# Performance work log

Measured on AMD Instinct MI355X. Metric: run time of the kernel, lower is better.

Reference implementation:

```python
import jax, jax.numpy as jnp
import numpy as np

N_NODES = 100000
N_EDGES = 1600000
D = 128
N_LAYERS = 3
N_GRAPHS = 128


def setup_inputs() -> dict:
    key = jax.random.key(0)
    ks = jax.random.split(key, 8)
    x = jax.random.normal(ks[0], (N_NODES, D), dtype=jnp.float32)
    # stacked GIN-MLP params (all layers are D->D since hidden_dim == in_dim)
    scale = 1.0 / np.sqrt(D)
    W1 = jax.random.normal(ks[1], (N_LAYERS, D, D), dtype=jnp.float32) * scale
    b1 = jax.random.normal(ks[2], (N_LAYERS, D), dtype=jnp.float32) * 0.01
    W2 = jax.random.normal(ks[3], (N_LAYERS, D, D), dtype=jnp.float32) * scale
    b2 = jax.random.normal(ks[4], (N_LAYERS, D), dtype=jnp.float32) * 0.01
    edge_index = jax.random.randint(ks[5], (2, N_EDGES), 0, N_NODES, dtype=jnp.int64)
    batch = jnp.sort(jax.random.randint(ks[6], (N_NODES,), 0, N_GRAPHS, dtype=jnp.int64))
    return {"x": x, "W1": W1, "b1": b1, "W2": W2, "b2": b2,
            "edge_index": edge_index, "batch": batch}


def reference(x, W1, b1, W2, b2, edge_index, batch):
    src = edge_index[0]
    dst = edge_index[1]
    n = x.shape[0]
    eps = jnp.float32(0.0)  # GIN eps (PyG default, not trained)
    for i in range(N_LAYERS):
        # gather neighbor features along edges, scatter-add to destination nodes
        agg = jax.ops.segment_sum(x[src], dst, num_segments=n)  # [N, D]
        h = (1.0 + eps) * x + agg
        h = jax.nn.relu(h @ W1[i] + b1[i])
        x = h @ W2[i] + b2[i]
    # sum-pool readout per graph
    h_G = jax.ops.segment_sum(x, batch, num_segments=N_GRAPHS)  # [G, D]
    return h_G
```

## Files before the change

kernel.cpp:

```cpp
#include <hip/hip_runtime.h>
#include <hip/hip_bf16.h>
#include <stdint.h>

#define N_NODES 100000
#define N_EDGES 1600000
#define DIM 128
#define N_GRAPHS 128
#define LDA 136

#define NBKT 196
#define BCAP 12288
#define BP   10240
#define IDXCAP 2048

typedef unsigned int uint32;
typedef unsigned short ushort16;

typedef __bf16 bf16x8 __attribute__((ext_vector_type(8)));
typedef float fx4 __attribute__((ext_vector_type(4)));

__device__ __forceinline__ float bfLo(uint32 u){ return __builtin_bit_cast(float, (uint32)(u << 16)); }
__device__ __forceinline__ float bfHi(uint32 u){ return __builtin_bit_cast(float, (uint32)(u & 0xFFFF0000u)); }
__device__ __forceinline__ ushort16 f2bf(float f){
  uint32 u = __builtin_bit_cast(uint32, f);
  u = u + 0x7FFFu + ((u >> 16) & 1u);
  return (ushort16)(u >> 16);
}
__device__ __forceinline__ uint32 pack2(float a, float b){
  return (uint32)f2bf(a) | ((uint32)f2bf(b) << 16);
}

__global__ __launch_bounds__(256) void k_cvt_x(const float* __restrict__ x, ushort16* __restrict__ P,
                                               ushort16* __restrict__ Q){
  if (blockIdx.x == 6250){
    int t = threadIdx.x;
    uint4 z = {0u,0u,0u,0u};
    if (t < 16)                *(uint4*)(P + (size_t)N_NODES*128 + t*8)      = z;
    else if (t < 32)           *(uint4*)(Q + (size_t)N_NODES*128 + (t-16)*8) = z;
    return;
  }
  int idx = (blockIdx.x*256 + threadIdx.x) * 8;
  float4 v0 = *(const float4*)(x + idx);
  float4 v1 = *(const float4*)(x + idx + 4);
  uint4 o;
  o.x = pack2(v0.x, v0.y); o.y = pack2(v0.z, v0.w);
  o.z = pack2(v1.x, v1.y); o.w = pack2(v1.z, v1.w);
  *(uint4*)(P + idx) = o;
}

__global__ __launch_bounds__(256) void k_cvt_w(const float* __restrict__ W1, const float* __restrict__ W2,
                                               ushort16* __restrict__ Wf){
  int tid = blockIdx.x*256 + threadIdx.x;
  int layer = tid >> 12;
  int rem   = tid & 4095;
  int mat   = rem >> 11;
  int nt    = (rem >> 8) & 7;
  int kt    = (rem >> 6) & 3;
  int lane  = rem & 63;
  int kg = lane >> 4, m = lane & 15;
  int n  = nt*16 + m;
  int kb = kt*32 + kg*8;
  const float* src = (mat ? W2 : W1) + layer*16384;
  uint4 o;
  o.x = pack2(src[(kb+0)*128 + n], src[(kb+1)*128 + n]);
  o.y = pack2(src[(kb+2)*128 + n], src[(kb+3)*128 + n]);
  o.z = pack2(src[(kb+4)*128 + n], src[(kb+5)*128 + n]);
  o.w = pack2(src[(kb+6)*128 + n], src[(kb+7)*128 + n]);
  *(uint4*)(Wf + ((((size_t)(layer*2+mat)*8 + nt)*4 + kt)*64 + lane)*8) = o;
}

__global__ __launch_bounds__(512) void k_binA(const int* __restrict__ ei,
                                              int* __restrict__ bucketCursor,
                                              int* __restrict__ temp){
  __shared__ int hist[NBKT];
  __shared__ int base[NBKT];
  __shared__ int gbase[NBKT];
  __shared__ int scanbuf[256];
  __shared__ int sVal[8192];
  __shared__ unsigned short sBkt[8192];
  int t = threadIdx.x;
  int e0 = blockIdx.x * 8192;

  for (int i = t; i < NBKT; i += 512) hist[i] = 0;
  __syncthreads();

  int   myv[16];
  short myb[16];
  short myr[16];
  #pragma unroll
  for (int it = 0; it < 16; ++it){
    int e = e0 + it*512 + t;
    int v = 0; short b = -1; short r = 0;
    if (e < N_EDGES){
      int s = ei[e];
      int d = ei[N_EDGES + e];
      b = (short)(d >> 9);
      v = s | ((d & 511) << 17);
      r = (short)atomicAdd(&hist[b], 1);
    }
    myv[it] = v; myb[it] = b; myr[it] = r;
  }
  __syncthreads();

  if (t < 256) scanbuf[t] = (t < NBKT) ? hist[t] : 0;
  __syncthreads();
  for (int off = 1; off < 256; off <<= 1){
    int x = 0;
    if (t < 256 && t >= off) x = scanbuf[t - off];
    __syncthreads();
    if (t < 256) scanbuf[t] += x;
    __syncthreads();
  }
  if (t < NBKT){
    base[t]  = scanbuf[t] - hist[t];
    gbase[t] = atomicAdd(&bucketCursor[t], hist[t]);
  }
  __syncthreads();

  #pragma unroll
  for (int it = 0; it < 16; ++it){
    if (myb[it] >= 0){
      int p = base[myb[it]] + myr[it];
      sVal[p] = myv[it];
      sBkt[p] = (unsigned short)myb[it];
    }
  }
  __syncthreads();

  int cnt = scanbuf[NBKT - 1];
  for (int p = t; p < cnt; p += 512){
    int b = sBkt[p];
    int g = gbase[b] + (p - base[b]);
    if (g < BCAP) temp[b*BCAP + g] = sVal[p];
  }
}

__global__ __launch_bounds__(512) void k_binB(const int* __restrict__ temp,
                                              const int* __restrict__ bucketCursor,
                                              int* __restrict__ rowptr,
                                              int* __restrict__ rowlen,
                                              int* __restrict__ colx){
  __shared__ int counts[512];
  __shared__ int sc[512];
  __shared__ int cur[512];
  __shared__ int stage[BCAP];
  __shared__ int sorted[BCAP];
  int b = blockIdx.x, t = threadIdx.x;
  int cnt = min(bucketCursor[b], BCAP);
  int gb  = b * BP;
  const int* src = temp + b*BCAP;

  counts[t] = 0;
  __syncthreads();
  for (int p = t; p < cnt; p += 512){
    int v = src[p];
    stage[p] = v;
    atomicAdd(&counts[v >> 17], 1);
  }
  __syncthreads();

  int len  = counts[t];
  int plen = (len + 3) & ~3;
  sc[t] = plen; __syncthreads();
  for (int off = 1; off < 512; off <<= 1){
    int x = (t >= off) ? sc[t - off] : 0; __syncthreads(); sc[t] += x; __syncthreads();
  }
  int excl = sc[t] - plen;
  cur[t] = excl;
  int node = b*512 + t;
  if (node < N_NODES){ rowptr[node] = gb + excl; rowlen[node] = plen; }
  __syncthreads();

  for (int p = t; p < cnt; p += 512){
    int v = stage[p];
    int d = v >> 17;
    int pos = atomicAdd(&cur[d], 1);
    sorted[pos] = v & 0x1FFFF;
  }
  __syncthreads();

  for (int k = len; k < plen; ++k) sorted[excl + k] = N_NODES;
  __syncthreads();

  int total = sc[511];
  for (int p = t; p < total; p += 512) colx[gb + p] = sorted[p];
}

__global__ __launch_bounds__(256, 6) void k_gin(const ushort16* __restrict__ xb, ushort16* __restrict__ hb,
                                                const ushort16* __restrict__ Wt1, const float* __restrict__ b1,
                                                const ushort16* __restrict__ Wt2, const float* __restrict__ b2,
                                                const int* __restrict__ rowptr, const int* __restrict__ rowlen,
                                                const int* __restrict__ colx){
  __shared__ __attribute__((aligned(16))) ushort16 sA[64 * LDA];
  __shared__ __attribute__((aligned(16))) int sIdx[IDXCAP];
  __shared__ int sOff[64];
  __shared__ int sLen[64];

  int t = threadIdx.x;
  int row0 = blockIdx.x * 64;
  int jBase = rowptr[row0];
  int lastV = min(row0 + 63, N_NODES - 1);
  int total = rowptr[lastV] + rowlen[lastV] - jBase;

  if (t < 64){
    int g = row0 + t;
    int off = 0, len = 0;
    if (g < N_NODES){ off = rowptr[g] - jBase; len = rowlen[g]; }
    sOff[t] = off; sLen[t] = len;
  }
  bool fast = (total <= IDXCAP);
  if (fast){
    for (int p = t; p < total; p += 256) sIdx[p] = colx[jBase + p];
  }
  __syncthreads();

  int wave = t >> 6, lane = t & 63;
  int g16 = lane >> 4, o = lane & 15;
  const uint32* xw = (const uint32*)xb;

#define GATH(r) (*(const uint4*)(xw + (size_t)(r)*64 + o*4))
#define ACC8(u) do { \
    a0 += (fx4){ bfLo((u).x), bfHi((u).x), bfLo((u).y), bfHi((u).y) }; \
    a1 += (fx4){ bfLo((u).z), bfHi((u).z), bfLo((u).w), bfHi((u).w) }; \
  } while(0)

  for (int q = 0; q < 4; ++q){
    int ln  = wave*16 + q*4 + g16;
    int off = sOff[ln];
    int len = sLen[ln];
    int gn  = row0 + ln;
    uint4 xv = {0u,0u,0u,0u};
    if (gn < N_NODES) xv = *(const uint4*)(xw + (size_t)gn*64 + o*4);
    fx4 a0 = (fx4){0.f,0.f,0.f,0.f};
    fx4 a1 = (fx4){0.f,0.f,0.f,0.f};

    if (fast){
      int rd = 0;
      for (; rd + 8 <= len; rd += 8){
        int i0 = sIdx[off+rd  ], i1 = sIdx[off+rd+1], i2 = sIdx[off+rd+2], i3 = sIdx[off+rd+3];
        int i4 = sIdx[off+rd+4], i5 = sIdx[off+rd+5], i6 = sIdx[off+rd+6], i7 = sIdx[off+rd+7];
        uint4 u0 = GATH(i0); uint4 u1 = GATH(i1); uint4 u2 = GATH(i2); uint4 u3 = GATH(i3);
        uint4 u4 = GATH(i4); uint4 u5 = GATH(i5); uint4 u6 = GATH(i6); uint4 u7 = GATH(i7);
        ACC8(u0); ACC8(u1); ACC8(u2); ACC8(u3);
        ACC8(u4); ACC8(u5); ACC8(u6); ACC8(u7);
      }
      if (rd < len){
        int i0 = sIdx[off+rd], i1 = sIdx[off+rd+1], i2 = sIdx[off+rd+2], i3 = sIdx[off+rd+3];
        uint4 u0 = GATH(i0); uint4 u1 = GATH(i1); uint4 u2 = GATH(i2); uint4 u3 = GATH(i3);
        ACC8(u0); ACC8(u1); ACC8(u2); ACC8(u3);
      }
    } else {
      for (int rd = 0; rd < len; rd += 4){
        int i0 = colx[jBase+off+rd], i1 = colx[jBase+off+rd+1];
        int i2 = colx[jBase+off+rd+2], i3 = colx[jBase+off+rd+3];
        uint4 u0 = GATH(i0); uint4 u1 = GATH(i1); uint4 u2 = GATH(i2); uint4 u3 = GATH(i3);
        ACC8(u0); ACC8(u1); ACC8(u2); ACC8(u3);
      }
    }

    uint4 r;
    r.x = pack2(a0[0]+bfLo(xv.x), a0[1]+bfHi(xv.x));
    r.y = pack2(a0[2]+bfLo(xv.y), a0[3]+bfHi(xv.y));
    r.z = pack2(a1[0]+bfLo(xv.z), a1[1]+bfHi(xv.z));
    r.w = pack2(a1[2]+bfLo(xv.w), a1[3]+bfHi(xv.w));
    *(uint4*)(sA + ln*LDA + o*8) = r;
  }
#undef GATH
#undef ACC8
  __syncthreads();

  int m = lane & 15, kg = lane >> 4;
  int n0 = wave * 2;

  bf16x8 bfa[4], bfb[4];
  #pragma unroll
  for (int kt = 0; kt < 4; ++kt){
    bfa[kt] = *(const bf16x8*)(Wt1 + (((n0+0)*4 + kt)*64 + lane)*8);
    bfb[kt] = *(const bf16x8*)(Wt1 + (((n0+1)*4 + kt)*64 + lane)*8);
  }

  fx4 acc[4][2];
  #pragma unroll
  for (int mt = 0; mt < 4; ++mt){ acc[mt][0] = (fx4){0,0,0,0}; acc[mt][1] = (fx4){0,0,0,0}; }

  #pragma unroll
  for (int kt = 0; kt < 4; ++kt){
    #pragma unroll
    for (int mt = 0; mt < 4; ++mt){
      bf16x8 av = *(const bf16x8*)(sA + (mt*16 + m)*LDA + kg*8 + kt*32);
      acc[mt][0] = __builtin_amdgcn_mfma_f32_16x16x32_bf16(av, bfa[kt], acc[mt][0], 0, 0, 0);
      acc[mt][1] = __builtin_amdgcn_mfma_f32_16x16x32_bf16(av, bfb[kt], acc[mt][1], 0, 0, 0);
    }
  }
  float bva = b1[(n0+0)*16 + m];
  float bvb = b1[(n0+1)*16 + m];
  __syncthreads();

  #pragma unroll
  for (int mt = 0; mt < 4; ++mt){
    #pragma unroll
    for (int r = 0; r < 4; ++r){
      int row = mt*16 + kg*4 + r;
      sA[row*LDA + (n0+0)*16 + m] = f2bf(fmaxf(acc[mt][0][r] + bva, 0.f));
      sA[row*LDA + (n0+1)*16 + m] = f2bf(fmaxf(acc[mt][1][r] + bvb, 0.f));
    }
  }
  #pragma unroll
  for (int kt = 0; kt < 4; ++kt){
    bfa[kt] = *(const bf16x8*)(Wt2 + (((n0+0)*4 + kt)*64 + lane)*8);
    bfb[kt] = *(const bf16x8*)(Wt2 + (((n0+1)*4 + kt)*64 + lane)*8);
  }
  float cva = b2[(n0+0)*16 + m];
  float cvb = b2[(n0+1)*16 + m];
  #pragma unroll
  for (int mt = 0; mt < 4; ++mt){ acc[mt][0] = (fx4){0,0,0,0}; acc[mt][1] = (fx4){0,0,0,0}; }
  __syncthreads();

  #pragma unroll
  for (int kt = 0; kt < 4; ++kt){
    #pragma unroll
    for (int mt = 0; mt < 4; ++mt){
      bf16x8 av = *(const bf16x8*)(sA + (mt*16 + m)*LDA + kg*8 + kt*32);
      acc[mt][0] = __builtin_amdgcn_mfma_f32_16x16x32_bf16(av, bfa[kt], acc[mt][0], 0, 0, 0);
      acc[mt][1] = __builtin_amdgcn_mfma_f32_16x16x32_bf16(av, bfb[kt], acc[mt][1], 0, 0, 0);
    }
  }

  #pragma unroll
  for (int mt = 0; mt < 4; ++mt){
    #pragma unroll
    for (int r = 0; r < 4; ++r){
      int row = row0 + mt*16 + kg*4 + r;
      if (row < N_NODES){
        hb[row*128 + (n0+0)*16 + m] = f2bf(acc[mt][0][r] + cva);
        hb[row*128 + (n0+1)*16 + m] = f2bf(acc[mt][1][r] + cvb);
      }
    }
  }
}

__device__ __forceinline__ int lower_bound_i(const int* __restrict__ a, int n, int key){
  int lo = 0, hi = n;
  while (lo < hi){ int mid = (lo + hi) >> 1; if (a[mid] < key) lo = mid + 1; else hi = mid; }
  return lo;
}

__global__ __launch_bounds__(256) void k_pool(const ushort16* __restrict__ xb, const int* __restrict__ batch,
                                              float* __restrict__ out){
  int g = blockIdx.x >> 2;
  int p = blockIdx.x & 3;
  int start = lower_bound_i(batch, N_NODES, g);
  int end   = lower_bound_i(batch, N_NODES, g + 1);
  int t = threadIdx.x;
  int c = t & 127;
  int h = t >> 7;
  float acc = 0.f;
  for (int r = start + p*2 + h; r < end; r += 8){
    uint32 u = (uint32)xb[r*128 + c];
    acc += __builtin_bit_cast(float, (uint32)(u << 16));
  }
  __shared__ float red[256];
  red[t] = acc; __syncthreads();
  if (t < 128) atomicAdd(&out[g*128 + c], red[t] + red[t + 128]);
}

extern "C" void kernel_launch(void* const* d_in, const int* in_sizes, int n_in,
                              void* d_out, int out_size, void* d_ws, size_t ws_size,
                              hipStream_t stream) {
  const float* x   = (const float*)d_in[0];
  const float* W1  = (const float*)d_in[1];
  const float* b1  = (const float*)d_in[2];
  const float* W2  = (const float*)d_in[3];
  const float* b2  = (const float*)d_in[4];
  const int*   ei  = (const int*)d_in[5];
  const int*   bat = (const int*)d_in[6];
  float* out = (float*)d_out;

  char* w = (char*)d_ws;
  auto carve = [&](size_t bytes) -> char* {
    char* p = w; w += (bytes + 255) & ~(size_t)255; return p;
  };
  ushort16* P    = (ushort16*)carve((size_t)(N_NODES+1) * DIM * 2);
  ushort16* Q    = (ushort16*)carve((size_t)(N_NODES+1) * DIM * 2);
  ushort16* Wf   = (ushort16*)carve((size_t)3 * 2 * 16384 * 2);
  int* rowptr    = (int*)carve((size_t)N_NODES * 4);
  int* rowlen    = (int*)carve((size_t)N_NODES * 4);
  int* colx      = (int*)carve((size_t)NBKT * BP * 4);
  int* bucketCursor = (int*)carve((NBKT + 1) * 4);
  int* temp      = (int*)Q;

  hipMemsetAsync(bucketCursor, 0, (NBKT + 1) * 4, stream);
  hipMemsetAsync(d_out, 0, (size_t)N_GRAPHS * DIM * 4, stream);

  k_cvt_x<<<6251, 256, 0, stream>>>(x, P, Q);
  k_cvt_w<<<48, 256, 0, stream>>>(W1, W2, Wf);

  k_binA<<<(N_EDGES + 8191)/8192, 512, 0, stream>>>(ei, bucketCursor, temp);
  k_binB<<<NBKT, 512, 0, stream>>>(temp, bucketCursor, rowptr, rowlen, colx);

  const int ginGrid = (N_NODES + 63) / 64;

  k_gin<<<ginGrid, 256, 0, stream>>>(P, Q, Wf + 0*16384, b1 + 0*128, Wf + 1*16384, b2 + 0*128,
                                     rowptr, rowlen, colx);
  k_gin<<<ginGrid, 256, 0, stream>>>(Q, P, Wf + 2*16384, b1 + 1*128, Wf + 3*16384, b2 + 1*128,
                                     rowptr, rowlen, colx);
  k_gin<<<ginGrid, 256, 0, stream>>>(P, Q, Wf + 4*16384, b1 + 2*128, Wf + 5*16384, b2 + 2*128,
                                     rowptr, rowlen, colx);

  k_pool<<<N_GRAPHS * 4, 256, 0, stream>>>(Q, bat, out);
}
```

Before: 372.9 us.

## Fuse x/W conversion and edge binning into one prep kernel, halve bucket size

Merges the x-to-bf16 conversion, weight repacking and first edge-binning pass into a single launch with block-range dispatch, removing two kernel launches and letting the independent work run concurrently. The destination bucketing is also refined from 512-node to 256-node buckets (392 buckets, smaller per-bucket capacity), so the second binning pass has more, smaller blocks with lighter shared-memory use. The trade-offs are smaller overflow headroom per bucket and more global atomics on the bucket cursors.

```diff
diff --git a/kernel.cpp b/kernel.cpp
--- a/kernel.cpp
+++ b/kernel.cpp
@@ -8,10 +8,13 @@
 #define N_GRAPHS 128
 #define LDA 136
 
-#define NBKT 196
-#define BCAP 12288
-#define BP   10240
+#define NBKT 392
+#define BCAP 6144
+#define BP   5632
 #define IDXCAP 2048
+
+#define NBIN_BLK 391
+#define CVT_BLK 3125
 
 typedef unsigned int uint32;
 typedef unsigned short ushort16;
@@ -30,27 +33,99 @@
   return (uint32)f2bf(a) | ((uint32)f2bf(b) << 16);
 }
 
-__global__ __launch_bounds__(256) void k_cvt_x(const float* __restrict__ x, ushort16* __restrict__ P,
-                                               ushort16* __restrict__ Q){
-  if (blockIdx.x == 6250){
-    int t = threadIdx.x;
+__global__ __launch_bounds__(512) void k_prep(const float* __restrict__ x,
+                                              const float* __restrict__ W1, const float* __restrict__ W2,
+                                              const int* __restrict__ ei,
+                                              ushort16* __restrict__ P, ushort16* __restrict__ Q,
+                                              ushort16* __restrict__ Wf,
+                                              int* __restrict__ bucketCursor,
+                                              int* __restrict__ temp){
+  __shared__ int hist[NBKT];
+  __shared__ int base[NBKT];
+  __shared__ int gbase[NBKT];
+  __shared__ int scanbuf[512];
+  __shared__ int sVal[4096];
+  __shared__ unsigned short sBkt[4096];
+
+  int bb = blockIdx.x;
+  int t  = threadIdx.x;
+
+  if (bb < NBIN_BLK){
+    int e0 = bb * 4096;
+    for (int i = t; i < NBKT; i += 512) hist[i] = 0;
+    __syncthreads();
+
+    int   myv[8];
+    short myb[8];
+    short myr[8];
+    #pragma unroll
+    for (int it = 0; it < 8; ++it){
+      int e = e0 + it*512 + t;
+      int v = 0; short b = -1; short r = 0;
+      if (e < N_EDGES){
+        int s = ei[e];
+        int d = ei[N_EDGES + e];
+        b = (short)(d >> 8);
+        v = s | ((d & 255) << 17);
+        r = (short)atomicAdd(&hist[b], 1);
+      }
+      myv[it] = v; myb[it] = b; myr[it] = r;
+    }
+    __syncthreads();
+
+    scanbuf[t] = (t < NBKT) ? hist[t] : 0;
+    __syncthreads();
+    for (int off = 1; off < 512; off <<= 1){
+      int x2 = 0;
+      if (t >= off) x2 = scanbuf[t - off];
+      __syncthreads();
+      scanbuf[t] += x2;
+      __syncthreads();
+    }
+    if (t < NBKT){
+      base[t]  = scanbuf[t] - hist[t];
+      gbase[t] = atomicAdd(&bucketCursor[t], hist[t]);
+    }
+    __syncthreads();
+
+    #pragma unroll
+    for (int it = 0; it < 8; ++it){
+      if (myb[it] >= 0){
+        int p = base[myb[it]] + myr[it];
+        sVal[p] = myv[it];
+        sBkt[p] = (unsigned short)myb[it];
+      }
+    }
+    __syncthreads();
+
+    int cnt = scanbuf[NBKT - 1];
+    for (int p = t; p < cnt; p += 512){
+      int b = sBkt[p];
+      int g = gbase[b] + (p - base[b]);
+      if (g < BCAP) temp[b*BCAP + g] = sVal[p];
+    }
+    return;
+  }
+
+  if (bb < NBIN_BLK + CVT_BLK){
+    int idx = ((bb - NBIN_BLK)*512 + t) * 8;
+    float4 v0 = *(const float4*)(x + idx);
+    float4 v1 = *(const float4*)(x + idx + 4);
+    uint4 o;
+    o.x = pack2(v0.x, v0.y); o.y = pack2(v0.z, v0.w);
+    o.z = pack2(v1.x, v1.y); o.w = pack2(v1.z, v1.w);
+    *(uint4*)(P + idx) = o;
+    return;
+  }
+
+  if (bb == NBIN_BLK + CVT_BLK){
     uint4 z = {0u,0u,0u,0u};
     if (t < 16)                *(uint4*)(P + (size_t)N_NODES*128 + t*8)      = z;
     else if (t < 32)           *(uint4*)(Q + (size_t)N_NODES*128 + (t-16)*8) = z;
     return;
   }
-  int idx = (blockIdx.x*256 + threadIdx.x) * 8;
-  float4 v0 = *(const float4*)(x + idx);
-  float4 v1 = *(const float4*)(x + idx + 4);
-  uint4 o;
-  o.x = pack2(v0.x, v0.y); o.y = pack2(v0.z, v0.w);
-  o.z = pack2(v1.x, v1.y); o.w = pack2(v1.z, v1.w);
-  *(uint4*)(P + idx) = o;
-}
-
-__global__ __launch_bounds__(256) void k_cvt_w(const float* __restrict__ W1, const float* __restrict__ W2,
-                                               ushort16* __restrict__ Wf){
-  int tid = blockIdx.x*256 + threadIdx.x;
+
+  int tid = (bb - (NBIN_BLK + CVT_BLK + 1))*512 + t;
   int layer = tid >> 12;
   int rem   = tid & 4095;
   int mat   = rem >> 11;
@@ -69,80 +144,14 @@
   *(uint4*)(Wf + ((((size_t)(layer*2+mat)*8 + nt)*4 + kt)*64 + lane)*8) = o;
 }
 
-__global__ __launch_bounds__(512) void k_binA(const int* __restrict__ ei,
-                                              int* __restrict__ bucketCursor,
-                                              int* __restrict__ temp){
-  __shared__ int hist[NBKT];
-  __shared__ int base[NBKT];
-  __shared__ int gbase[NBKT];
-  __shared__ int scanbuf[256];
-  __shared__ int sVal[8192];
-  __shared__ unsigned short sBkt[8192];
-  int t = threadIdx.x;
-  int e0 = blockIdx.x * 8192;
-
-  for (int i = t; i < NBKT; i += 512) hist[i] = 0;
-  __syncthreads();
-
-  int   myv[16];
-  short myb[16];
-  short myr[16];
-  #pragma unroll
-  for (int it = 0; it < 16; ++it){
-    int e = e0 + it*512 + t;
-    int v = 0; short b = -1; short r = 0;
-    if (e < N_EDGES){
-      int s = ei[e];
-      int d = ei[N_EDGES + e];
-      b = (short)(d >> 9);
-      v = s | ((d & 511) << 17);
-      r = (short)atomicAdd(&hist[b], 1);
-    }
-    myv[it] = v; myb[it] = b; myr[it] = r;
-  }
-  __syncthreads();
-
-  if (t < 256) scanbuf[t] = (t < NBKT) ? hist[t] : 0;
-  __syncthreads();
-  for (int off = 1; off < 256; off <<= 1){
-    int x = 0;
-    if (t < 256 && t >= off) x = scanbuf[t - off];
-    __syncthreads();
-    if (t < 256) scanbuf[t] += x;
-    __syncthreads();
-  }
-  if (t < NBKT){
-    base[t]  = scanbuf[t] - hist[t];
-    gbase[t] = atomicAdd(&bucketCursor[t], hist[t]);
-  }
-  __syncthreads();
-
-  #pragma unroll
-  for (int it = 0; it < 16; ++it){
-    if (myb[it] >= 0){
-      int p = base[myb[it]] + myr[it];
-      sVal[p] = myv[it];
-      sBkt[p] = (unsigned short)myb[it];
-    }
-  }
-  __syncthreads();
-
-  int cnt = scanbuf[NBKT - 1];
-  for (int p = t; p < cnt; p += 512){
-    int b = sBkt[p];
-    int g = gbase[b] + (p - base[b]);
-    if (g < BCAP) temp[b*BCAP + g] = sVal[p];
-  }
-}
-
 __global__ __launch_bounds__(512) void k_binB(const int* __restrict__ temp,
                                               const int* __restrict__ bucketCursor,
                                               int* __restrict__ rowptr,
                                               int* __restrict__ rowlen,
                                               int* __restrict__ colx){
-  __shared__ int counts[512];
-  __shared__ int sc[512];
-  __shared__ int cur[512];
+  __shared__ int counts[256];
+  __shared__ int sc[256];
+  __shared__ int cur[256];
   __shared__ int stage[BCAP];
   __shared__ int sorted[BCAP];
   int b = blockIdx.x, t = threadIdx.x;
@@ -150,7 +159,7 @@
   int gb  = b * BP;
   const int* src = temp + b*BCAP;
 
-  counts[t] = 0;
+  if (t < 256) counts[t] = 0;
   __syncthreads();
   for (int p = t; p < cnt; p += 512){
     int v = src[p];
@@ -159,16 +168,27 @@
   }
   __syncthreads();
 
-  int len  = counts[t];
-  int plen = (len + 3) & ~3;
-  sc[t] = plen; __syncthreads();
-  for (int off = 1; off < 512; off <<= 1){
-    int x = (t >= off) ? sc[t - off] : 0; __syncthreads(); sc[t] += x; __syncthreads();
-  }
-  int excl = sc[t] - plen;
-  cur[t] = excl;
-  int node = b*512 + t;
-  if (node < N_NODES){ rowptr[node] = gb + excl; rowlen[node] = plen; }
+  int len = 0, plen = 0;
+  if (t < 256){
+    len  = counts[t];
+    plen = (len + 3) & ~3;
+    sc[t] = plen;
+  }
+  __syncthreads();
+  for (int off = 1; off < 256; off <<= 1){
+    int x = 0;
+    if (t < 256 && t >= off) x = sc[t - off];
+    __syncthreads();
+    if (t < 256) sc[t] += x;
+    __syncthreads();
+  }
+  int excl = 0;
+  if (t < 256){
+    excl = sc[t] - plen;
+    cur[t] = excl;
+    int node = b*256 + t;
+    if (node < N_NODES){ rowptr[node] = gb + excl; rowlen[node] = plen; }
+  }
   __syncthreads();
 
   for (int p = t; p < cnt; p += 512){
@@ -179,10 +199,12 @@
   }
   __syncthreads();
 
-  for (int k = len; k < plen; ++k) sorted[excl + k] = N_NODES;
-  __syncthreads();
-
-  int total = sc[511];
+  if (t < 256){
+    for (int k = len; k < plen; ++k) sorted[excl + k] = N_NODES;
+  }
+  __syncthreads();
+
+  int total = min(sc[255], BP);
   for (int p = t; p < total; p += 512) colx[gb + p] = sorted[p];
 }
 
@@ -392,10 +414,8 @@
   hipMemsetAsync(bucketCursor, 0, (NBKT + 1) * 4, stream);
   hipMemsetAsync(d_out, 0, (size_t)N_GRAPHS * DIM * 4, stream);
 
-  k_cvt_x<<<6251, 256, 0, stream>>>(x, P, Q);
-  k_cvt_w<<<48, 256, 0, stream>>>(W1, W2, Wf);
-
-  k_binA<<<(N_EDGES + 8191)/8192, 512, 0, stream>>>(ei, bucketCursor, temp);
+  k_prep<<<NBIN_BLK + CVT_BLK + 1 + 24, 512, 0, stream>>>(x, W1, W2, ei, P, Q, Wf,
+                                                          bucketCursor, temp);
   k_binB<<<NBKT, 512, 0, stream>>>(temp, bucketCursor, rowptr, rowlen, colx);
 
   const int ginGrid = (N_NODES + 63) / 64;
```

Result: faster. 358.9 us (-3.8%).
